# Optimization experiments

Measured on AMD Instinct MI355X. Metric: run time of the kernel, lower is better.

## Reference

```python
import jax, jax.numpy as jnp
import numpy as np

B, N, C = 2, 2048, 768
H = 12
HD = C // H
SCALE = HD ** -0.5


def setup_inputs() -> dict:
    key = jax.random.key(0)
    ks = jax.random.split(key, 5)
    s = 1.0 / np.sqrt(C)
    return {
        "x": jax.random.normal(ks[0], (B, N, C), dtype=jnp.float32),
        "Wq": jax.random.normal(ks[1], (C, C), dtype=jnp.float32) * s,
        "Wk": jax.random.normal(ks[2], (C, C), dtype=jnp.float32) * s,
        "Wv": jax.random.normal(ks[3], (C, C), dtype=jnp.float32) * s,
        "Wo": jax.random.normal(ks[4], (C, C), dtype=jnp.float32) * s,
        "bo": jnp.zeros((C,), dtype=jnp.float32),
    }


def reference(x, Wq, Wk, Wv, Wo, bo):
    b, n, c = x.shape
    # projections (equinox Linear: y = W @ x, i.e. x @ W.T); split heads -> [b, h, n, hd]
    q = (x @ Wq.T).reshape(b, n, H, HD).transpose(0, 2, 1, 3)
    k = (x @ Wk.T).reshape(b, n, H, HD).transpose(0, 2, 1, 3)
    v = (x @ Wv.T).reshape(b, n, H, HD).transpose(0, 2, 1, 3)
    # full O(N^2) score matrix, scaled dot-product
    scores = jnp.einsum("bhqd,bhkd->bhqk", q, k) * SCALE  # [b, h, n, n]
    probs = jax.nn.softmax(scores, axis=-1)
    # attn_drop = 0.0 -> identity
    out = jnp.einsum("bhqk,bhkd->bhqd", probs, v)  # [b, h, n, hd]
    out = out.transpose(0, 2, 1, 3).reshape(b, n, c)
    # output projection (proj_drop = 0.0 -> identity)
    return out @ Wo.T + bo
```

## Files before the change

kernel.cpp:

```cpp
#include <hip/hip_runtime.h>
#include <hip/hip_bf16.h>
#include <cstdint>

typedef __bf16 bf16;
typedef bf16 bf16x8 __attribute__((ext_vector_type(8)));
typedef float f32x4 __attribute__((ext_vector_type(4)));
typedef uint32_t u32;

#define MFMA16(a, b, c) __builtin_amdgcn_mfma_f32_16x16x32_bf16(a, b, c, 0, 0, 0)

static constexpr int Bb = 2, Hh = 12, Nn = 2048, Cc = 768, HD = 64;
static constexpr float SCALE = 0.125f;
static constexpr float LOG2E = 1.4426950408889634f;

__device__ inline u32 pkbf(float a, float b) {
    union { struct { uint16_t lo, hi; } s; u32 w; } u;
    u.s.lo = __builtin_bit_cast(uint16_t, (bf16)a);
    u.s.hi = __builtin_bit_cast(uint16_t, (bf16)b);
    return u.w;
}

__device__ __forceinline__ size_t fidx(int bh, int n, int hd) {
    return ((size_t)(bh * 128 + (n >> 4)) * 2 + (hd >> 5)) * 512 +
           (size_t)(((hd >> 3) & 3) * 128 + (n & 15) * 8 + (hd & 7));
}
__device__ __forceinline__ size_t vidx(int bh, int n, int hd) {
    return (((size_t)(bh * 32 + (n >> 6)) * 4 + (hd >> 4)) * 2 + ((n >> 5) & 1)) * 512 +
           (size_t)(((n >> 3) & 3) * 128 + (hd & 15) * 8 + (n & 7));
}

__device__ __forceinline__ void stage16(const bf16* g, bf16* l) {
    __builtin_amdgcn_global_load_lds(
        (const __attribute__((address_space(1))) void*)g,
        (__attribute__((address_space(3))) void*)l, 16, 0, 0);
}

__global__ __launch_bounds__(256) void cvt_f32_bf16(const float* __restrict__ in,
                                                    bf16* __restrict__ out, int n8) {
    int i = blockIdx.x * blockDim.x + threadIdx.x;
    if (i >= n8) return;
    const float4* p = reinterpret_cast<const float4*>(in) + (size_t)i * 2;
    float4 v0 = p[0], v1 = p[1];
    bf16x8 o;
    o[0] = (bf16)v0.x; o[1] = (bf16)v0.y; o[2] = (bf16)v0.z; o[3] = (bf16)v0.w;
    o[4] = (bf16)v1.x; o[5] = (bf16)v1.y; o[6] = (bf16)v1.z; o[7] = (bf16)v1.w;
    reinterpret_cast<bf16x8*>(out)[i] = o;
}

__global__ __launch_bounds__(256) void cvt4_f32_bf16(const float* __restrict__ s0, const float* __restrict__ s1,
                                                     const float* __restrict__ s2, const float* __restrict__ s3,
                                                     bf16* __restrict__ d0, bf16* __restrict__ d1,
                                                     bf16* __restrict__ d2, bf16* __restrict__ d3, int n8) {
    int i = blockIdx.x * blockDim.x + threadIdx.x;
    if (i >= n8) return;
    const float* in = blockIdx.y == 0 ? s0 : blockIdx.y == 1 ? s1 : blockIdx.y == 2 ? s2 : s3;
    bf16* out = blockIdx.y == 0 ? d0 : blockIdx.y == 1 ? d1 : blockIdx.y == 2 ? d2 : d3;
    const float4* p = reinterpret_cast<const float4*>(in) + (size_t)i * 2;
    float4 v0 = p[0], v1 = p[1];
    bf16x8 o;
    o[0] = (bf16)v0.x; o[1] = (bf16)v0.y; o[2] = (bf16)v0.z; o[3] = (bf16)v0.w;
    o[4] = (bf16)v1.x; o[5] = (bf16)v1.y; o[6] = (bf16)v1.z; o[7] = (bf16)v1.w;
    reinterpret_cast<bf16x8*>(out)[i] = o;
}

__global__ __launch_bounds__(256) void gemm_qkv(const bf16* __restrict__ X,
                                                const bf16* __restrict__ W,
                                                bf16* __restrict__ QF,
                                                bf16* __restrict__ KF,
                                                bf16* __restrict__ VF) {
    const int m0  = blockIdx.x * 128;
    const int grp = blockIdx.y / 12;
    const int j0  = (blockIdx.y % 12) * 64;
    const int j00 = blockIdx.y * 64;
    const int w   = threadIdx.x >> 6;
    const int l   = threadIdx.x & 63;
    const int lr  = l & 15;
    const int lg  = l >> 4;

    __shared__ bf16 lsA[2][128 * 32];
    __shared__ bf16 lsB[2][64 * 32];

    const int lrow = l >> 2;
    const int lcol = (l & 3) * 8;

    auto STAGE = [&](int buf, int kk) {
#pragma unroll
        for (int i = 0; i < 2; i++) {
            const int s = w * 2 + i;
            stage16(X + (size_t)(m0 + s * 16 + lrow) * Cc + kk + lcol, &lsA[buf][s * 512]);
        }
        stage16(W + (size_t)(j00 + w * 16 + lrow) * Cc + kk + lcol, &lsB[buf][w * 512]);
    };

    f32x4 acc[2][4] = {};

    STAGE(0, 0);
    __syncthreads();
    int cur = 0;
#pragma unroll 1
    for (int it = 0; it < 24; ++it) {
        if (it < 23) STAGE(cur ^ 1, (it + 1) * 32);
        bf16x8 a[2], b[4];
#pragma unroll
        for (int r = 0; r < 2; r++)
            a[r] = *reinterpret_cast<const bf16x8*>(&lsA[cur][(w * 32 + r * 16 + lr) * 32 + lg * 8]);
#pragma unroll
        for (int c = 0; c < 4; c++)
            b[c] = *reinterpret_cast<const bf16x8*>(&lsB[cur][(c * 16 + lr) * 32 + lg * 8]);
        __builtin_amdgcn_s_setprio(1);
#pragma unroll
        for (int r = 0; r < 2; r++)
#pragma unroll
            for (int c = 0; c < 4; c++)
                acc[r][c] = MFMA16(a[r], b[c], acc[r][c]);
        __builtin_amdgcn_s_setprio(0);
        __syncthreads();
        cur ^= 1;
    }

    const int mw = m0 + w * 32;
#pragma unroll
    for (int r = 0; r < 2; r++)
#pragma unroll
        for (int c = 0; c < 4; c++)
#pragma unroll
            for (int j = 0; j < 4; j++) {
                const int m   = mw + r * 16 + lg * 4 + j;
                const int col = j0 + c * 16 + lr;
                const int bb = m >> 11, n = m & 2047;
                const int h = col >> 6, hd = col & 63;
                const int bh = bb * Hh + h;
                const float v = acc[r][c][j];
                if (grp == 0) {
                    QF[fidx(bh, n, hd)] = (bf16)(v * SCALE);
                } else if (grp == 1) {
                    KF[fidx(bh, n, hd)] = (bf16)v;
                } else {
                    VF[vidx(bh, n, hd)] = (bf16)v;
                }
            }
}

__global__ __launch_bounds__(256) void gemm_proj(const bf16* __restrict__ X,
                                                 const bf16* __restrict__ W,
                                                 const float* __restrict__ bias,
                                                 float* __restrict__ Y) {
    const int m0 = blockIdx.x * 64;
    const int j0 = blockIdx.y * 64;
    const int w  = threadIdx.x >> 6;
    const int l  = threadIdx.x & 63;
    const int lr = l & 15;
    const int lg = l >> 4;

    __shared__ bf16 lsA[2][64 * 32];
    __shared__ bf16 lsB[2][64 * 32];

    const int lrow = l >> 2;
    const int lcol = (l & 3) * 8;

    auto STAGE = [&](int buf, int kk) {
        stage16(X + (size_t)(m0 + w * 16 + lrow) * Cc + kk + lcol, &lsA[buf][w * 512]);
        stage16(W + (size_t)(j0 + w * 16 + lrow) * Cc + kk + lcol, &lsB[buf][w * 512]);
    };

    f32x4 acc[4] = {};

    STAGE(0, 0);
    __syncthreads();
    int cur = 0;
#pragma unroll 1
    for (int it = 0; it < 24; ++it) {
        if (it < 23) STAGE(cur ^ 1, (it + 1) * 32);
        bf16x8 a = *reinterpret_cast<const bf16x8*>(&lsA[cur][(w * 16 + lr) * 32 + lg * 8]);
        bf16x8 b[4];
#pragma unroll
        for (int c = 0; c < 4; c++)
            b[c] = *reinterpret_cast<const bf16x8*>(&lsB[cur][(c * 16 + lr) * 32 + lg * 8]);
        __builtin_amdgcn_s_setprio(1);
#pragma unroll
        for (int c = 0; c < 4; c++)
            acc[c] = MFMA16(a, b[c], acc[c]);
        __builtin_amdgcn_s_setprio(0);
        __syncthreads();
        cur ^= 1;
    }

    const int mw = m0 + w * 16;
#pragma unroll
    for (int c = 0; c < 4; c++)
#pragma unroll
        for (int j = 0; j < 4; j++) {
            const int m   = mw + lg * 4 + j;
            const int col = j0 + c * 16 + lr;
            Y[(size_t)m * Cc + col] = acc[c][j] + bias[col];
        }
}

__global__ __launch_bounds__(256, 3) void attn_kernel(const bf16* __restrict__ QF,
                                                      const bf16* __restrict__ KF,
                                                      const bf16* __restrict__ VF,
                                                      bf16* __restrict__ AO) {
    const int bid = (blockIdx.x & 7) * 96 + (blockIdx.x >> 3);
    const int qb  = bid & 31;
    const int bh  = bid >> 5;
    const int tid = threadIdx.x;
    const int wid = tid >> 6;
    const int l   = tid & 63;
    const int lr  = l & 15;
    const int lg  = l >> 4;

    __shared__ bf16 kv[2][8192];
    __shared__ u32  p_lds[4][16 * 36];

    f32x4 acc[4] = {};
    float rsum = 0.f;

    const bf16* Qp = QF + ((size_t)(bh * 128 + qb * 4 + wid) * 2) * 512 + l * 8;
    const bf16x8 qf0 = *reinterpret_cast<const bf16x8*>(Qp);
    const bf16x8 qf1 = *reinterpret_cast<const bf16x8*>(Qp + 512);

    auto STAGE = [&](int buf, int t) {
        const size_t tb = ((size_t)bh * 256 + t * 8) * 512;
#pragma unroll
        for (int i = 0; i < 4; i++) {
            const int s = wid * 4 + i;
            const bf16* src = (s < 8 ? KF + tb + (size_t)s * 512
                                     : VF + tb + (size_t)(s - 8) * 512) + l * 8;
            stage16(src, &kv[buf][s * 512]);
        }
    };

    const f32x4 fz = {0.f, 0.f, 0.f, 0.f};

    STAGE(0, 0);
    __syncthreads();
    int cur = 0;

#pragma unroll 1
    for (int t = 0; t < 32; ++t) {
        if (t < 31) STAGE(cur ^ 1, t + 1);

        bf16x8 kf[8];
#pragma unroll
        for (int s8 = 0; s8 < 8; s8++)
            kf[s8] = *reinterpret_cast<const bf16x8*>(&kv[cur][s8 * 512 + l * 8]);
        f32x4 s[4];
        __builtin_amdgcn_s_setprio(1);
#pragma unroll
        for (int st = 0; st < 4; st++) {
            s[st] = MFMA16(kf[st * 2], qf0, fz);
            s[st] = MFMA16(kf[st * 2 + 1], qf1, s[st]);
        }
        __builtin_amdgcn_s_setprio(0);

        float p[4][4];
#pragma unroll
        for (int st = 0; st < 4; st++)
#pragma unroll
            for (int j = 0; j < 4; j++) {
                p[st][j] = exp2f(s[st][j] * LOG2E);
                rsum += p[st][j];
            }
#pragma unroll
        for (int st = 0; st < 4; st++) {
            u32 w0 = pkbf(p[st][0], p[st][1]);
            u32 w1 = pkbf(p[st][2], p[st][3]);
            *reinterpret_cast<uint2*>(&p_lds[wid][lr * 36 + st * 8 + lg * 2]) = make_uint2(w0, w1);
        }
        asm volatile("s_waitcnt lgkmcnt(0)" ::: "memory");
        __builtin_amdgcn_sched_barrier(0);
        const bf16x8 pa0 = *reinterpret_cast<const bf16x8*>(&p_lds[wid][lr * 36 + lg * 4]);
        const bf16x8 pa1 = *reinterpret_cast<const bf16x8*>(&p_lds[wid][lr * 36 + 16 + lg * 4]);

        bf16x8 vf[8];
#pragma unroll
        for (int s8 = 0; s8 < 8; s8++)
            vf[s8] = *reinterpret_cast<const bf16x8*>(&kv[cur][(8 + s8) * 512 + l * 8]);
        __builtin_amdgcn_s_setprio(1);
#pragma unroll
        for (int c = 0; c < 4; c++) {
            acc[c] = MFMA16(vf[c * 2], pa0, acc[c]);
            acc[c] = MFMA16(vf[c * 2 + 1], pa1, acc[c]);
        }
        __builtin_amdgcn_s_setprio(0);

        __syncthreads();
        cur ^= 1;
    }

    rsum += __shfl_xor(rsum, 16);
    rsum += __shfl_xor(rsum, 32);

    float* o_lds = reinterpret_cast<float*>(&kv[0][0]) + wid * 1088;
    const float rinv = 1.0f / rsum;
#pragma unroll
    for (int c = 0; c < 4; c++)
#pragma unroll
        for (int j = 0; j < 4; j++)
            o_lds[(c * 16 + lg * 4 + j) * 17 + lr] = acc[c][j] * rinv;
    asm volatile("s_waitcnt lgkmcnt(0)" ::: "memory");
    __builtin_amdgcn_sched_barrier(0);

    const int bb = bh / Hh, h = bh % Hh;
    const int q0 = qb * 64 + wid * 16;
    const int qq = l >> 2, dc = (l & 3) * 16;
    bf16x8 o0, o1;
#pragma unroll
    for (int dd = 0; dd < 8; dd++) o0[dd] = (bf16)o_lds[(dc + dd) * 17 + qq];
#pragma unroll
    for (int dd = 0; dd < 8; dd++) o1[dd] = (bf16)o_lds[(dc + 8 + dd) * 17 + qq];
    bf16* dst = AO + ((size_t)(bb * Nn) + q0 + qq) * Cc + h * 64 + dc;
    *reinterpret_cast<bf16x8*>(dst) = o0;
    *reinterpret_cast<bf16x8*>(dst + 8) = o1;
}

extern "C" void kernel_launch(void* const* d_in, const int* in_sizes, int n_in,
                              void* d_out, int out_size, void* d_ws, size_t ws_size,
                              hipStream_t stream) {
    const float* x  = (const float*)d_in[0];
    const float* Wq = (const float*)d_in[1];
    const float* Wk = (const float*)d_in[2];
    const float* Wv = (const float*)d_in[3];
    const float* Wo = (const float*)d_in[4];
    const float* bo = (const float*)d_in[5];

    const size_t XB    = 0;
    const size_t WQKVB = XB + 6291456;
    const size_t WOB   = WQKVB + 3538944;
    const size_t QB    = WOB + 1179648;
    const size_t KB    = QB + 6291456;
    const size_t VTB   = KB + 6291456;
    const size_t AOB   = VTB + 6291456;
    const size_t NEED  = AOB + 6291456;
    if (ws_size < NEED) return;

    char* ws = (char*)d_ws;
    bf16* xb   = (bf16*)(ws + XB);
    bf16* wqkv = (bf16*)(ws + WQKVB);
    bf16* wob  = (bf16*)(ws + WOB);
    bf16* QF   = (bf16*)(ws + QB);
    bf16* KF   = (bf16*)(ws + KB);
    bf16* VF   = (bf16*)(ws + VTB);
    bf16* AOb  = (bf16*)(ws + AOB);

    cvt_f32_bf16<<<1536, 256, 0, stream>>>(x, xb, (Bb * Nn * Cc) / 8);
    cvt4_f32_bf16<<<dim3(288, 4), 256, 0, stream>>>(Wq, Wk, Wv, Wo,
                                                    wqkv, wqkv + 589824, wqkv + 1179648, wob,
                                                    (Cc * Cc) / 8);

    gemm_qkv<<<dim3(32, 36), 256, 0, stream>>>(xb, wqkv, QF, KF, VF);

    attn_kernel<<<768, 256, 0, stream>>>(QF, KF, VF, AOb);

    gemm_proj<<<dim3(64, 12), 256, 0, stream>>>(AOb, wob, bo, (float*)d_out);
}
```

Baseline: 109.1 us.

## Split K/V staging with vmcnt waits in attention and enlarge QKV GEMM tile

The attention kernel now stages K and V separately. K is double-buffered and V single-buffered, and fine-grained vmcnt waits with raw barriers replace one syncthreads per tile, so V loads overlap the QK and softmax phases and LDS use shrinks enough to allow 4 blocks per CU. The QKV GEMM moves from 128x64 to 128x128 tiles using a 2x2 wave layout, which raises MFMA reuse per LDS load but halves the grid. The hand-counted vmcnt values are a correctness risk if the load accounting is wrong.

```diff
diff --git a/kernel.cpp b/kernel.cpp
--- a/kernel.cpp
+++ b/kernel.cpp
@@ -34,6 +34,9 @@
         (const __attribute__((address_space(1))) void*)g,
         (__attribute__((address_space(3))) void*)l, 16, 0, 0);
 }
+
+#define VMWAIT(N) do { asm volatile("s_waitcnt vmcnt(" #N ")" ::); \
+                       __builtin_amdgcn_sched_barrier(0); } while (0)
 
 __global__ __launch_bounds__(256) void cvt_f32_bf16(const float* __restrict__ in,
                                                     bf16* __restrict__ out, int n8) {
@@ -63,22 +66,24 @@
     reinterpret_cast<bf16x8*>(out)[i] = o;
 }
 
-__global__ __launch_bounds__(256) void gemm_qkv(const bf16* __restrict__ X,
-                                                const bf16* __restrict__ W,
-                                                bf16* __restrict__ QF,
-                                                bf16* __restrict__ KF,
-                                                bf16* __restrict__ VF) {
-    const int m0  = blockIdx.x * 128;
-    const int grp = blockIdx.y / 12;
-    const int j0  = (blockIdx.y % 12) * 64;
-    const int j00 = blockIdx.y * 64;
+__global__ __launch_bounds__(256, 3) void gemm_qkv(const bf16* __restrict__ X,
+                                                   const bf16* __restrict__ W,
+                                                   bf16* __restrict__ QF,
+                                                   bf16* __restrict__ KF,
+                                                   bf16* __restrict__ VF) {
+    const int m0      = blockIdx.x * 128;
+    const int j00     = blockIdx.y * 128;
+    const int grp     = blockIdx.y / 6;
+    const int colbase = (blockIdx.y % 6) * 128;
     const int w   = threadIdx.x >> 6;
+    const int wr  = w >> 1;
+    const int wc  = w & 1;
     const int l   = threadIdx.x & 63;
     const int lr  = l & 15;
     const int lg  = l >> 4;
 
     __shared__ bf16 lsA[2][128 * 32];
-    __shared__ bf16 lsB[2][64 * 32];
+    __shared__ bf16 lsB[2][128 * 32];
 
     const int lrow = l >> 2;
     const int lcol = (l & 3) * 8;
@@ -88,11 +93,11 @@
         for (int i = 0; i < 2; i++) {
             const int s = w * 2 + i;
             stage16(X + (size_t)(m0 + s * 16 + lrow) * Cc + kk + lcol, &lsA[buf][s * 512]);
-        }
-        stage16(W + (size_t)(j00 + w * 16 + lrow) * Cc + kk + lcol, &lsB[buf][w * 512]);
-    };
-
-    f32x4 acc[2][4] = {};
+            stage16(W + (size_t)(j00 + s * 16 + lrow) * Cc + kk + lcol, &lsB[buf][s * 512]);
+        }
+    };
+
+    f32x4 acc[4][4] = {};
 
     STAGE(0, 0);
     __syncthreads();
@@ -100,16 +105,16 @@
 #pragma unroll 1
     for (int it = 0; it < 24; ++it) {
         if (it < 23) STAGE(cur ^ 1, (it + 1) * 32);
-        bf16x8 a[2], b[4];
-#pragma unroll
-        for (int r = 0; r < 2; r++)
-            a[r] = *reinterpret_cast<const bf16x8*>(&lsA[cur][(w * 32 + r * 16 + lr) * 32 + lg * 8]);
+        bf16x8 a[4], b[4];
+#pragma unroll
+        for (int r = 0; r < 4; r++)
+            a[r] = *reinterpret_cast<const bf16x8*>(&lsA[cur][(wr * 64 + r * 16 + lr) * 32 + lg * 8]);
 #pragma unroll
         for (int c = 0; c < 4; c++)
-            b[c] = *reinterpret_cast<const bf16x8*>(&lsB[cur][(c * 16 + lr) * 32 + lg * 8]);
+            b[c] = *reinterpret_cast<const bf16x8*>(&lsB[cur][(wc * 64 + c * 16 + lr) * 32 + lg * 8]);
         __builtin_amdgcn_s_setprio(1);
 #pragma unroll
-        for (int r = 0; r < 2; r++)
+        for (int r = 0; r < 4; r++)
 #pragma unroll
             for (int c = 0; c < 4; c++)
                 acc[r][c] = MFMA16(a[r], b[c], acc[r][c]);
@@ -118,15 +123,14 @@
         cur ^= 1;
     }
 
-    const int mw = m0 + w * 32;
-#pragma unroll
-    for (int r = 0; r < 2; r++)
+#pragma unroll
+    for (int r = 0; r < 4; r++)
 #pragma unroll
         for (int c = 0; c < 4; c++)
 #pragma unroll
             for (int j = 0; j < 4; j++) {
-                const int m   = mw + r * 16 + lg * 4 + j;
-                const int col = j0 + c * 16 + lr;
+                const int m   = m0 + wr * 64 + r * 16 + lg * 4 + j;
+                const int col = colbase + wc * 64 + c * 16 + lr;
                 const int bb = m >> 11, n = m & 2047;
                 const int h = col >> 6, hd = col & 63;
                 const int bh = bb * Hh + h;
@@ -196,7 +200,7 @@
         }
 }
 
-__global__ __launch_bounds__(256, 3) void attn_kernel(const bf16* __restrict__ QF,
+__global__ __launch_bounds__(256, 4) void attn_kernel(const bf16* __restrict__ QF,
                                                       const bf16* __restrict__ KF,
                                                       const bf16* __restrict__ VF,
                                                       bf16* __restrict__ AO) {
@@ -209,7 +213,7 @@
     const int lr  = l & 15;
     const int lg  = l >> 4;
 
-    __shared__ bf16 kv[2][8192];
+    __shared__ bf16 kvbuf[3 * 4096];
     __shared__ u32  p_lds[4][16 * 36];
 
     f32x4 acc[4] = {};
@@ -219,32 +223,30 @@
     const bf16x8 qf0 = *reinterpret_cast<const bf16x8*>(Qp);
     const bf16x8 qf1 = *reinterpret_cast<const bf16x8*>(Qp + 512);
 
-    auto STAGE = [&](int buf, int t) {
+    auto STAGE_K = [&](int buf, int t) {
         const size_t tb = ((size_t)bh * 256 + t * 8) * 512;
 #pragma unroll
-        for (int i = 0; i < 4; i++) {
-            const int s = wid * 4 + i;
-            const bf16* src = (s < 8 ? KF + tb + (size_t)s * 512
-                                     : VF + tb + (size_t)(s - 8) * 512) + l * 8;
-            stage16(src, &kv[buf][s * 512]);
+        for (int i = 0; i < 2; i++) {
+            const int s = wid * 2 + i;
+            stage16(KF + tb + (size_t)s * 512 + l * 8, &kvbuf[buf * 4096 + s * 512]);
+        }
+    };
+    auto STAGE_V = [&](int t) {
+        const size_t tb = ((size_t)bh * 256 + t * 8) * 512;
+#pragma unroll
+        for (int i = 0; i < 2; i++) {
+            const int s = wid * 2 + i;
+            stage16(VF + tb + (size_t)s * 512 + l * 8, &kvbuf[8192 + s * 512]);
         }
     };
 
     const f32x4 fz = {0.f, 0.f, 0.f, 0.f};
 
-    STAGE(0, 0);
-    __syncthreads();
-    int cur = 0;
-
-#pragma unroll 1
-    for (int t = 0; t < 32; ++t) {
-        if (t < 31) STAGE(cur ^ 1, t + 1);
-
+    auto QKPHASE = [&](int cur, f32x4* s) {
         bf16x8 kf[8];
 #pragma unroll
         for (int s8 = 0; s8 < 8; s8++)
-            kf[s8] = *reinterpret_cast<const bf16x8*>(&kv[cur][s8 * 512 + l * 8]);
-        f32x4 s[4];
+            kf[s8] = *reinterpret_cast<const bf16x8*>(&kvbuf[cur * 4096 + s8 * 512 + l * 8]);
         __builtin_amdgcn_s_setprio(1);
 #pragma unroll
         for (int st = 0; st < 4; st++) {
@@ -252,7 +254,8 @@
             s[st] = MFMA16(kf[st * 2 + 1], qf1, s[st]);
         }
         __builtin_amdgcn_s_setprio(0);
-
+    };
+    auto SOFTMAX = [&](f32x4* s, bf16x8& pa0, bf16x8& pa1) {
         float p[4][4];
 #pragma unroll
         for (int st = 0; st < 4; st++)
@@ -269,13 +272,14 @@
         }
         asm volatile("s_waitcnt lgkmcnt(0)" ::: "memory");
         __builtin_amdgcn_sched_barrier(0);
-        const bf16x8 pa0 = *reinterpret_cast<const bf16x8*>(&p_lds[wid][lr * 36 + lg * 4]);
-        const bf16x8 pa1 = *reinterpret_cast<const bf16x8*>(&p_lds[wid][lr * 36 + 16 + lg * 4]);
-
+        pa0 = *reinterpret_cast<const bf16x8*>(&p_lds[wid][lr * 36 + lg * 4]);
+        pa1 = *reinterpret_cast<const bf16x8*>(&p_lds[wid][lr * 36 + 16 + lg * 4]);
+    };
+    auto PVPHASE = [&](const bf16x8& pa0, const bf16x8& pa1) {
         bf16x8 vf[8];
 #pragma unroll
         for (int s8 = 0; s8 < 8; s8++)
-            vf[s8] = *reinterpret_cast<const bf16x8*>(&kv[cur][(8 + s8) * 512 + l * 8]);
+            vf[s8] = *reinterpret_cast<const bf16x8*>(&kvbuf[8192 + s8 * 512 + l * 8]);
         __builtin_amdgcn_s_setprio(1);
 #pragma unroll
         for (int c = 0; c < 4; c++) {
@@ -283,15 +287,45 @@
             acc[c] = MFMA16(vf[c * 2 + 1], pa1, acc[c]);
         }
         __builtin_amdgcn_s_setprio(0);
-
-        __syncthreads();
+    };
+
+    STAGE_K(0, 0);
+    STAGE_V(0);
+    int cur = 0;
+
+#pragma unroll 1
+    for (int t = 0; t < 31; ++t) {
+        VMWAIT(2);
+        __builtin_amdgcn_s_barrier();
+        f32x4 s[4];
+        QKPHASE(cur, s);
+        STAGE_K(cur ^ 1, t + 1);
+        bf16x8 pa0, pa1;
+        SOFTMAX(s, pa0, pa1);
+        VMWAIT(2);
+        __builtin_amdgcn_s_barrier();
+        PVPHASE(pa0, pa1);
+        __builtin_amdgcn_s_barrier();
+        STAGE_V(t + 1);
         cur ^= 1;
     }
+    VMWAIT(2);
+    __builtin_amdgcn_s_barrier();
+    {
+        f32x4 s[4];
+        QKPHASE(cur, s);
+        bf16x8 pa0, pa1;
+        SOFTMAX(s, pa0, pa1);
+        VMWAIT(0);
+        __builtin_amdgcn_s_barrier();
+        PVPHASE(pa0, pa1);
+    }
+    __builtin_amdgcn_s_barrier();
 
     rsum += __shfl_xor(rsum, 16);
     rsum += __shfl_xor(rsum, 32);
 
-    float* o_lds = reinterpret_cast<float*>(&kv[0][0]) + wid * 1088;
+    float* o_lds = reinterpret_cast<float*>(&kvbuf[0]) + wid * 1088;
     const float rinv = 1.0f / rsum;
 #pragma unroll
     for (int c = 0; c < 4; c++)
@@ -348,7 +382,7 @@
                                                     wqkv, wqkv + 589824, wqkv + 1179648, wob,
                                                     (Cc * Cc) / 8);
 
-    gemm_qkv<<<dim3(32, 36), 256, 0, stream>>>(xb, wqkv, QF, KF, VF);
+    gemm_qkv<<<dim3(32, 18), 256, 0, stream>>>(xb, wqkv, QF, KF, VF);
 
     attn_kernel<<<768, 256, 0, stream>>>(QF, KF, VF, AOb);
 
```

Measured after the change: 105.8 us. 1.03x faster.
